# Kernel tuning notes

Hardware: AMD Instinct MI355X
Metric: run time of the kernel (lower is better)

Reference implementation:

```python
import jax, jax.numpy as jnp
import numpy as np
from jax import lax

B, N, C = 4, 16384, 256
NH, HD = 8, 32          # num_heads, head_dim
SR = 4                  # spatial reduction ratio
LMAX = 6144             # max per-batch query length (static pad size)
QLENS = np.array([2048, 6144, 3072, 5120], dtype=np.int32)
TQ = int(QLENS.sum())   # 16384 total ragged queries
SCALE = HD ** -0.5


def setup_inputs() -> dict:
    key = jax.random.key(0)
    ks = jax.random.split(key, 6)
    w = lambda k, s: jax.random.normal(k, s, jnp.float32) * 0.02
    return {
        "x": jax.random.normal(ks[0], (B, N, C), jnp.float32),
        "q": jax.random.normal(ks[1], (TQ, C), jnp.float32),
        "H": 128,
        "W": 128,
        "q_lengths": jnp.asarray(QLENS),
        "w_q": w(ks[2], (C, C)),        # stored [in, out] (= torch W.T)
        "w_kv": w(ks[3], (C, 2 * C)),
        "sr_w": w(ks[4], (C, C, SR, SR)),  # OIHW
        "sr_b": jnp.zeros((C,), jnp.float32),
        "ln_g": jnp.ones((C,), jnp.float32),
        "ln_b": jnp.zeros((C,), jnp.float32),
        "proj_w": w(ks[5], (C, C)),
        "proj_b": jnp.zeros((C,), jnp.float32),
    }


def reference(x, q, H, W, q_lengths, w_q, w_kv, sr_w, sr_b, ln_g, ln_b, proj_w, proj_b):
    # q projection -> per-head ragged queries [NH, TQ, HD]
    qh = (q @ w_q).reshape(TQ, NH, HD).transpose(1, 0, 2)

    # spatial reduction of KV source: conv(k=SR, stride=SR) + LayerNorm
    x_ = x.transpose(0, 2, 1).reshape(B, C, H, W)
    x_ = lax.conv_general_dilated(x_, sr_w, (SR, SR), "VALID",
                                  dimension_numbers=("NCHW", "OIHW", "NCHW"))
    x_ = x_ + sr_b[None, :, None, None]
    x_ = x_.reshape(B, C, -1).transpose(0, 2, 1)  # [B, Nkv, C]
    mu = x_.mean(-1, keepdims=True)
    var = ((x_ - mu) ** 2).mean(-1, keepdims=True)
    x_ = (x_ - mu) * lax.rsqrt(var + 1e-5) * ln_g + ln_b

    # kv projection -> [NH, B, Nkv, HD] each
    kv = (x_ @ w_kv).reshape(B, -1, 2, NH, HD)
    k = kv[:, :, 0].transpose(2, 0, 1, 3)
    v = kv[:, :, 1].transpose(2, 0, 1, 3)

    # ragged -> padded layout for the variable-length attention
    batch_ids = jnp.repeat(jnp.arange(B), q_lengths, total_repeat_length=TQ)
    offsets = jnp.cumsum(q_lengths) - q_lengths
    pos = jnp.arange(TQ) - offsets[batch_ids]
    qp = jnp.zeros((NH, B, LMAX, HD), qh.dtype).at[:, batch_ids, pos].set(qh)

    # per-batch attention over reduced keys (padded rows are discarded below)
    attn = jax.nn.softmax(jnp.einsum("hbld,hbkd->hblk", qp, k) * SCALE, axis=-1)
    op = jnp.einsum("hblk,hbkd->hbld", attn, v)

    # gather valid ragged outputs back: [NH, TQ, HD] -> [TQ, C]
    o = op[:, batch_ids, pos].transpose(1, 0, 2).reshape(TQ, C)
    return o @ proj_w + proj_b
```

## Files before the change

kernel.cpp:

```cpp
#include <hip/hip_runtime.h>
#include <hip/hip_bf16.h>


using bf16 = __hip_bfloat16;
using f32x4 = __attribute__((ext_vector_type(4))) float;
using bf16x8 = __attribute__((ext_vector_type(8))) short;

#define DEVINL __device__ __forceinline__
#define AS1 __attribute__((address_space(1)))
#define AS3 __attribute__((address_space(3)))

DEVINL f32x4 mfma16(bf16x8 a, bf16x8 b, f32x4 c) {
    return __builtin_amdgcn_mfma_f32_16x16x32_bf16(a, b, c, 0, 0, 0);
}

DEVINL unsigned short f2bf(float f) {
    union { float f; unsigned u; } x; x.f = f;
    unsigned u = x.u;
    u += 0x7fffu + ((u >> 16) & 1u);
    return (unsigned short)(u >> 16);
}

DEVINL unsigned pk_rtz(float a, float b) {
    return __builtin_amdgcn_perm(__float_as_uint(b), __float_as_uint(a), 0x07060302u);
}

DEVINL float ex2(float x) { return __builtin_amdgcn_exp2f(x); }

DEVINL void gl16(const bf16* g, bf16* l) {
    __builtin_amdgcn_global_load_lds(
        (const AS1 void*)(unsigned long long)(uintptr_t)g,
        (AS3 void*)(unsigned)(uintptr_t)l, 16, 0, 0);
}
DEVINL void gl16f(const float* g, float* l) {
    __builtin_amdgcn_global_load_lds(
        (const AS1 void*)(unsigned long long)(uintptr_t)g,
        (AS3 void*)(unsigned)(uintptr_t)l, 16, 0, 0);
}

__global__ __launch_bounds__(256) void prep_kernel(
    const float* __restrict__ w_q, const float* __restrict__ w_kv,
    const float* __restrict__ proj_w, const float* __restrict__ sr_w,
    const float* __restrict__ q,
    bf16* __restrict__ wqT, bf16* __restrict__ wkvT, bf16* __restrict__ wprT,
    bf16* __restrict__ wcv, bf16* __restrict__ q_bf)
{
    const int bb = blockIdx.x;
    if (bb < 256) {
        int idx = bb * 256 + threadIdx.x;
        int k = idx & 255, n = idx >> 8;
        wqT[idx] = __float2bfloat16(w_q[k * 256 + n]);
    } else if (bb < 768) {
        int idx = (bb - 256) * 256 + threadIdx.x;
        int k = idx & 255, n = idx >> 8;
        wkvT[idx] = __float2bfloat16(w_kv[k * 512 + n]);
    } else if (bb < 1024) {
        int idx = (bb - 768) * 256 + threadIdx.x;
        int k = idx & 255, n = idx >> 8;
        wprT[idx] = __float2bfloat16(proj_w[k * 256 + n]);
    } else if (bb < 5120) {
        int idx = (bb - 1024) * 256 + threadIdx.x;
        int o = idx >> 12, rest = idx & 4095, dydx = rest >> 8, c = rest & 255;
        wcv[idx] = __float2bfloat16(sr_w[((o << 8) + c) * 16 + dydx]);
    } else {
        int i = (bb - 5120) * 256 + threadIdx.x;
        float4 a = ((const float4*)q)[i * 2];
        float4 b = ((const float4*)q)[i * 2 + 1];
        uint4 u;
        u.x = f2bf(a.x) | ((unsigned)f2bf(a.y) << 16);
        u.y = f2bf(a.z) | ((unsigned)f2bf(a.w) << 16);
        u.z = f2bf(b.x) | ((unsigned)f2bf(b.y) << 16);
        u.w = f2bf(b.z) | ((unsigned)f2bf(b.w) << 16);
        ((uint4*)q_bf)[i] = u;
    }
}

template<int EMODE>
__global__ __launch_bounds__(256, 4) void gemm_kernel(
    const bf16* __restrict__ A, const bf16* __restrict__ WT,
    const float* __restrict__ bias,
    bf16* __restrict__ outb, float* __restrict__ outf, bf16* __restrict__ out2,
    int M, int N, int K, int KS)
{
    __shared__ alignas(16) bf16 As[2][64 * 64];
    __shared__ alignas(16) bf16 Bs[2][64 * 64];
    const int cpx = gridDim.x >> 3;
    const int bx = (blockIdx.x & 7) * cpx + (blockIdx.x >> 3);
    const int ntn = N >> 6;
    const int tm = bx / ntn, tn = bx % ntn;
    const int tid = threadIdx.x, lane = tid & 63, wid = tid >> 6;
    const int l15 = lane & 15, g = lane >> 4;
    const int wm = (wid >> 1) << 5, wn = (wid & 1) << 5;
    f32x4 acc[2][2] = {};

    int r_[2], cs_[2];
#pragma unroll
    for (int j = 0; j < 2; ++j) {
        int idx = (wid * 2 + j) * 64 + lane;
        r_[j] = idx >> 3;
        cs_[j] = ((idx & 7) ^ (r_[j] & 7)) << 3;
    }
    const bf16* Arow = &A[(size_t)(tm * 64) * K];
    const bf16* Brow = &WT[(size_t)(tn * 64) * K];

    const int kbeg = blockIdx.y * KS;
    const int nsteps = KS >> 6;

    auto stage = [&](int buf, int k0) {
#pragma unroll
        for (int j = 0; j < 2; ++j) {
            gl16(Arow + (size_t)r_[j] * K + (k0 + cs_[j]), &As[buf][(wid * 2 + j) * 512]);
            gl16(Brow + (size_t)r_[j] * K + (k0 + cs_[j]), &Bs[buf][(wid * 2 + j) * 512]);
        }
    };

    stage(0, kbeg);
    __syncthreads();

    for (int t = 0; t < nsteps; ++t) {
        const int buf = t & 1;
        if (t + 1 < nsteps) stage(buf ^ 1, kbeg + (t + 1) * 64);
#pragma unroll
        for (int kk = 0; kk < 2; ++kk) {
            const int sw = l15 & 7;
            const int co = ((kk * 4 + g) ^ sw) << 3;
            bf16x8 a0 = *(const bf16x8*)&As[buf][(wm + l15) * 64 + co];
            bf16x8 a1 = *(const bf16x8*)&As[buf][(wm + 16 + l15) * 64 + co];
            bf16x8 b0 = *(const bf16x8*)&Bs[buf][(wn + l15) * 64 + co];
            bf16x8 b1 = *(const bf16x8*)&Bs[buf][(wn + 16 + l15) * 64 + co];
            acc[0][0] = mfma16(a0, b0, acc[0][0]);
            acc[0][1] = mfma16(a0, b1, acc[0][1]);
            acc[1][0] = mfma16(a1, b0, acc[1][0]);
            acc[1][1] = mfma16(a1, b1, acc[1][1]);
        }
        __syncthreads();
    }

    const float qscale = 0.1767766953f * 1.4426950409f;
#pragma unroll
    for (int mi = 0; mi < 2; ++mi)
#pragma unroll
    for (int ni = 0; ni < 2; ++ni)
#pragma unroll
    for (int r = 0; r < 4; ++r) {
        int row = tm * 64 + wm + mi * 16 + g * 4 + r;
        int col = tn * 64 + wn + ni * 16 + l15;
        float v = acc[mi][ni][r];
        if constexpr (EMODE == 0) {
            outb[(size_t)row * 256 + col] = __float2bfloat16(v * qscale);
        } else if constexpr (EMODE == 1) {
            outf[(size_t)row * 256 + col] = v + bias[col];
        } else if constexpr (EMODE == 2) {
            int bb = row >> 10, key = row & 1023;
            if (col < 256) {
                int hh = col >> 5, d = col & 31;
                outb[(size_t)(((bb << 3) + hh) * 1024 + key) * 32 + d] = __float2bfloat16(v);
            } else {
                int d = col - 256;
                int c = key & 31;
                int pos = (((c >> 2) & 3) << 3) + ((c >> 4) << 2) + (c & 3);
                int keyp = (key & ~31) | pos;
                out2[(size_t)(((bb << 3) + (d >> 5)) * 32 + (d & 31)) * 1024 + keyp] =
                    __float2bfloat16(v);
            }
        }
    }
}

__global__ __launch_bounds__(1024, 4) void conv_gemm_kernel(
    const float* __restrict__ X, const bf16* __restrict__ WT,
    const float* __restrict__ bias, float* __restrict__ outf)
{
    __shared__ alignas(16) float Af[2][2][64 * 64];
    __shared__ alignas(16) bf16 Bs[2][2][64 * 64];
    const int K = 4096;
    const int bx = (blockIdx.x & 7) * 32 + (blockIdx.x >> 3);
    const int tm = bx >> 2, tn = bx & 3;
    const int tid = threadIdx.x, lane = tid & 63, wid = tid >> 6;
    const int grp = wid >> 3, wg = wid & 7;
    const int l15 = lane & 15, g = lane >> 4;
    const int wm = (wg >> 1) << 4, wn = (wg & 1) << 5;
    f32x4 acc[2] = {};

    size_t laneoffA[2];
#pragma unroll
    for (int j = 0; j < 2; ++j) {
        int rr = (wg * 2 + j) * 4 + (lane >> 4);
        int pr = tm * 64 + rr;
        int b = pr >> 10, pi = pr & 1023;
        int ii = pi >> 5, jj = pi & 31;
        int c16 = lane & 15;
        int c16s = ((((c16 >> 1) ^ (rr & 7)) << 1) | (c16 & 1));
        laneoffA[j] = ((size_t)((b << 14) + (ii << 2) * 128 + (jj << 2))) * 256
                      + c16s * 4;
    }
    const int rB = wg * 8 + (lane >> 3);
    const int csB = ((lane & 7) ^ (rB & 7)) << 3;
    const bf16* BrowP = &WT[(size_t)(tn * 64 + rB) * K + csB];

    const int kbeg = grp << 11;

    auto stage = [&](int buf, int t) {
        const int k0 = kbeg + t * 64;
        const int dydx = k0 >> 8;
        const int stepoff = ((dydx >> 2) * 128 + (dydx & 3)) * 256 + (k0 & 255);
#pragma unroll
        for (int j = 0; j < 2; ++j)
            gl16f(X + laneoffA[j] + stepoff, &Af[grp][buf][(wg * 2 + j) * 256]);
        gl16(BrowP + k0, &Bs[grp][buf][wg * 512]);
    };

    stage(0, 0);
    __syncthreads();

    for (int t = 0; t < 32; ++t) {
        const int buf = t & 1;
        if (t + 1 < 32) stage(buf ^ 1, t + 1);
#pragma unroll
        for (int kk = 0; kk < 2; ++kk) {
            const int sw = l15 & 7;
            const int uo = ((kk * 4 + g) ^ sw) << 3;
            const float* ap = &Af[grp][buf][(wm + l15) * 64 + uo];
            float4 lo = *(const float4*)ap;
            float4 hi = *(const float4*)(ap + 4);
            uint4 au;
            au.x = pk_rtz(lo.x, lo.y);  au.y = pk_rtz(lo.z, lo.w);
            au.z = pk_rtz(hi.x, hi.y);  au.w = pk_rtz(hi.z, hi.w);
            union { uint4 u; bf16x8 v; } ac; ac.u = au;
            bf16x8 b0 = *(const bf16x8*)&Bs[grp][buf][(wn + l15) * 64 + uo];
            bf16x8 b1 = *(const bf16x8*)&Bs[grp][buf][(wn + 16 + l15) * 64 + uo];
            acc[0] = mfma16(ac.v, b0, acc[0]);
            acc[1] = mfma16(ac.v, b1, acc[1]);
        }
        __syncthreads();
    }

    {
        float* red = &Af[grp][0][0];
#pragma unroll
        for (int ni = 0; ni < 2; ++ni)
#pragma unroll
        for (int r = 0; r < 4; ++r)
            red[(wm + g * 4 + r) * 64 + wn + ni * 16 + l15] = acc[ni][r];
    }
    __syncthreads();
    {
        const int e = tid << 2;
        const float4 s0 = *(const float4*)&Af[0][0][e];
        const float4 s1 = *(const float4*)&Af[1][0][e];
        const int row = e >> 6, col = e & 63;
        const float4 bv = *(const float4*)&bias[tn * 64 + col];
        float4 o;
        o.x = s0.x + s1.x + bv.x;
        o.y = s0.y + s1.y + bv.y;
        o.z = s0.z + s1.z + bv.z;
        o.w = s0.w + s1.w + bv.w;
        *(float4*)&outf[(size_t)(tm * 64 + row) * 256 + tn * 64 + col] = o;
    }
}

__global__ __launch_bounds__(256) void ln_kernel(const float* __restrict__ xr,
                                                 const float* __restrict__ gw,
                                                 const float* __restrict__ bw,
                                                 bf16* __restrict__ out) {
    int row = blockIdx.x * 4 + (threadIdx.x >> 6);
    int lane = threadIdx.x & 63;
    const float4 v = *(const float4*)&xr[(size_t)row * 256 + lane * 4];

    float s = v.x + v.y + v.z + v.w;
#pragma unroll
    for (int m = 1; m < 64; m <<= 1) s += __shfl_xor(s, m, 64);
    float mu = s * 0.00390625f;
    float d0 = v.x - mu, d1 = v.y - mu, d2 = v.z - mu, d3 = v.w - mu;
    float qv = d0 * d0 + d1 * d1 + d2 * d2 + d3 * d3;
#pragma unroll
    for (int m = 1; m < 64; m <<= 1) qv += __shfl_xor(qv, m, 64);
    float rstd = rsqrtf(qv * 0.00390625f + 1e-5f);
    const float4 gg = *(const float4*)&gw[lane * 4];
    const float4 bb = *(const float4*)&bw[lane * 4];
    uint2 u;
    u.x = f2bf(d0 * rstd * gg.x + bb.x) | ((unsigned)f2bf(d1 * rstd * gg.y + bb.y) << 16);
    u.y = f2bf(d2 * rstd * gg.z + bb.z) | ((unsigned)f2bf(d3 * rstd * gg.w + bb.w) << 16);
    *(uint2*)&out[(size_t)row * 256 + lane * 4] = u;
}

__global__ __launch_bounds__(256, 4) void attn_kernel(
    const bf16* __restrict__ qh, const bf16* __restrict__ kh,
    const bf16* __restrict__ vt, bf16* __restrict__ obf)
{
    __shared__ alignas(16) bf16 Kl[2][128 * 32];
    __shared__ alignas(16) bf16 Vl[2][32 * 128];
    const int bid = blockIdx.x;
    const int h = bid & 7;
    const int tile = bid >> 3;
    const int row0 = tile << 7;
    const int b = (row0 < 2048) ? 0 : (row0 < 8192) ? 1 : (row0 < 11264) ? 2 : 3;
    const int tid = threadIdx.x, lane = tid & 63, w = tid >> 6;
    const int l15 = lane & 15, g = lane >> 4;
    const int qbase = row0 + (w << 5);
    const int bh = (b << 3) + h;

    bf16x8 qfA = *(const bf16x8*)&qh[(size_t)(qbase + l15) * 256 + h * 32 + g * 8];
    bf16x8 qfB = *(const bf16x8*)&qh[(size_t)(qbase + 16 + l15) * 256 + h * 32 + g * 8];

    bf16x8 ones;
    {
        unsigned ov = (l15 == 0) ? 0x3f803f80u : 0u;
        unsigned* op = (unsigned*)&ones;
        op[0] = ov; op[1] = ov; op[2] = ov; op[3] = ov;
    }

    f32x4 o0A = {0.f,0.f,0.f,0.f}, o1A = o0A, o2A = o0A;
    f32x4 o0B = o0A, o1B = o0A, o2B = o0A;
    const f32x4 z = {0.f, 0.f, 0.f, 0.f};

    const int skey = lane >> 2;
    const int skc  = (lane & 3) ^ (skey & 3);
    const int svd  = lane >> 4;
    const int svc  = lane & 15;
    const bf16* kbase = kh + (size_t)bh * 1024 * 32;
    const bf16* vbase = vt + (size_t)bh * 32 * 1024;

    auto stage = [&](int buf, int kb) {
        if (w < 2) {
#pragma unroll
            for (int jj = 0; jj < 4; ++jj) {
                int j = w * 4 + jj;
                int key = (j << 4) + skey;
                gl16(kbase + (size_t)(kb + key) * 32 + (skc << 3), &Kl[buf][j * 512]);
            }
        } else {
#pragma unroll
            for (int jj = 0; jj < 4; ++jj) {
                int j = (w - 2) * 4 + jj;
                int d = (j << 2) + svd;
                gl16(vbase + (size_t)d * 1024 + kb + ((svc ^ (d & 7)) << 3),
                     &Vl[buf][j * 512]);
            }
        }
    };

    stage(0, 0);
    __syncthreads();

    const int kc = g ^ (l15 & 3);
    const int vsw = l15 & 7;

    for (int t = 0; t < 8; ++t) {
        const int buf = t & 1;
        if (t < 7) stage(buf ^ 1, (t + 1) << 7);
#pragma unroll
        for (int s = 0; s < 4; ++s) {
            bf16x8 k0 = *(const bf16x8*)&Kl[buf][((s << 5) + l15) * 32 + (kc << 3)];
            bf16x8 k1 = *(const bf16x8*)&Kl[buf][((s << 5) + 16 + l15) * 32 + (kc << 3)];
            bf16x8 v0 = *(const bf16x8*)&Vl[buf][(l15 << 7) + ((((s << 2) + g) ^ vsw) << 3)];
            bf16x8 v1 = *(const bf16x8*)&Vl[buf][((16 + l15) << 7) + ((((s << 2) + g) ^ vsw) << 3)];

            f32x4 s0A = mfma16(k0, qfA, z);
            f32x4 s1A = mfma16(k1, qfA, z);
            f32x4 s0B = mfma16(k0, qfB, z);
            f32x4 s1B = mfma16(k1, qfB, z);

            uint4 pAu, pBu;
            pAu.x = pk_rtz(ex2(s0A[0]), ex2(s0A[1]));
            pAu.y = pk_rtz(ex2(s0A[2]), ex2(s0A[3]));
            pAu.z = pk_rtz(ex2(s1A[0]), ex2(s1A[1]));
            pAu.w = pk_rtz(ex2(s1A[2]), ex2(s1A[3]));
            pBu.x = pk_rtz(ex2(s0B[0]), ex2(s0B[1]));
            pBu.y = pk_rtz(ex2(s0B[2]), ex2(s0B[3]));
            pBu.z = pk_rtz(ex2(s1B[0]), ex2(s1B[1]));
            pBu.w = pk_rtz(ex2(s1B[2]), ex2(s1B[3]));
            union { uint4 u; bf16x8 v; } cA, cB;
            cA.u = pAu; cB.u = pBu;

            o0A = mfma16(cA.v, v0, o0A);
            o1A = mfma16(cA.v, v1, o1A);
            o2A = mfma16(cA.v, ones, o2A);
            o0B = mfma16(cB.v, v0, o0B);
            o1B = mfma16(cB.v, v1, o1B);
            o2B = mfma16(cB.v, ones, o2B);
        }
        __syncthreads();
    }

#pragma unroll
    for (int r = 0; r < 4; ++r) {
        float invA = 1.f / __shfl(o2A[r], g << 4, 64);
        float invB = 1.f / __shfl(o2B[r], g << 4, 64);
        size_t orowA = (size_t)(qbase + (g << 2) + r) * 256 + h * 32;
        size_t orowB = (size_t)(qbase + 16 + (g << 2) + r) * 256 + h * 32;
        obf[orowA + l15]      = __float2bfloat16(o0A[r] * invA);
        obf[orowA + 16 + l15] = __float2bfloat16(o1A[r] * invA);
        obf[orowB + l15]      = __float2bfloat16(o0B[r] * invB);
        obf[orowB + 16 + l15] = __float2bfloat16(o1B[r] * invB);
    }
}


extern "C" void kernel_launch(void* const* d_in, const int* in_sizes, int n_in,
                              void* d_out, int out_size, void* d_ws, size_t ws_size,
                              hipStream_t stream)
{
    const float* x      = (const float*)d_in[0];
    const float* q      = (const float*)d_in[1];
    const float* w_q    = (const float*)d_in[5];
    const float* w_kv   = (const float*)d_in[6];
    const float* sr_w   = (const float*)d_in[7];
    const float* sr_b   = (const float*)d_in[8];
    const float* ln_g   = (const float*)d_in[9];
    const float* ln_b   = (const float*)d_in[10];
    const float* proj_w = (const float*)d_in[11];
    const float* proj_b = (const float*)d_in[12];

    char* w = (char*)d_ws;
    bf16* q_bf = (bf16*)(w + 0);
    bf16* qh   = (bf16*)(w + 8388608);
    bf16* wqT  = (bf16*)(w + 16777216);
    bf16* wkvT = (bf16*)(w + 16908288);
    bf16* wprT = (bf16*)(w + 17170432);
    bf16* wcv  = (bf16*)(w + 17301504);
    bf16* xln  = (bf16*)(w + 19398656);
    bf16* kh   = (bf16*)(w + 21495808);
    bf16* vt   = (bf16*)(w + 23592960);
    bf16* obf  = (bf16*)(w + 25690112);
    float* xr  = (float*)(w + 34078720);
    float* out = (float*)d_out;

    prep_kernel<<<7168, 256, 0, stream>>>(w_q, w_kv, proj_w, sr_w, q,
                                          wqT, wkvT, wprT, wcv, q_bf);
    gemm_kernel<0><<<1024, 256, 0, stream>>>(q_bf, wqT, nullptr, qh, nullptr, nullptr,
                                             16384, 256, 256, 256);
    conv_gemm_kernel<<<256, 1024, 0, stream>>>(x, wcv, sr_b, xr);
    ln_kernel<<<1024, 256, 0, stream>>>(xr, ln_g, ln_b, xln);
    gemm_kernel<2><<<512, 256, 0, stream>>>(xln, wkvT, nullptr, kh, nullptr, vt,
                                            4096, 512, 256, 256);
    attn_kernel<<<1024, 256, 0, stream>>>(qh, kh, vt, obf);
    gemm_kernel<1><<<1024, 256, 0, stream>>>(obf, wprT, proj_b, nullptr, out, nullptr,
                                             16384, 256, 256, 256);
}
```

Measured before the change: 95.33 us.

## Split-K conv GEMM into 8 slices with partial sums reduced in LayerNorm

The conv-as-GEMM kernel changes from 256 blocks of 1024 threads, which split K in two and reduced in shared memory, to 2048 blocks of 256 threads. Each block computes a 64x64 tile over one of 8 K-slices with a 32-wide K step and writes fp32 partials to workspace. The LayerNorm kernel now sums the 8 partials, adds the conv bias, then normalizes. This raises parallelism and occupancy on the many-CU GPU, at the cost of about 32MB of extra partial-sum traffic written and read back.

```diff
diff --git a/kernel.cpp b/kernel.cpp
--- a/kernel.cpp
+++ b/kernel.cpp
@@ -167,105 +167,107 @@
     }
 }
 
-__global__ __launch_bounds__(1024, 4) void conv_gemm_kernel(
+__global__ __launch_bounds__(256, 6) void conv_gemm_kernel(
     const float* __restrict__ X, const bf16* __restrict__ WT,
-    const float* __restrict__ bias, float* __restrict__ outf)
+    float* __restrict__ partials)
 {
-    __shared__ alignas(16) float Af[2][2][64 * 64];
-    __shared__ alignas(16) bf16 Bs[2][2][64 * 64];
+    __shared__ alignas(16) float Af[2][64 * 32];
+    __shared__ alignas(16) bf16 Bs[2][64 * 32];
     const int K = 4096;
-    const int bx = (blockIdx.x & 7) * 32 + (blockIdx.x >> 3);
-    const int tm = bx >> 2, tn = bx & 3;
+    const int swz = (blockIdx.x & 7) * 256 + (blockIdx.x >> 3);
+    const int combo = swz >> 6;
+    const int tm = swz & 63;
+    const int tn = combo >> 3, slice = combo & 7;
     const int tid = threadIdx.x, lane = tid & 63, wid = tid >> 6;
-    const int grp = wid >> 3, wg = wid & 7;
     const int l15 = lane & 15, g = lane >> 4;
-    const int wm = (wg >> 1) << 4, wn = (wg & 1) << 5;
-    f32x4 acc[2] = {};
+    const int wm = (wid >> 1) << 5, wn = (wid & 1) << 5;
+    f32x4 acc[2][2] = {};
 
     size_t laneoffA[2];
 #pragma unroll
     for (int j = 0; j < 2; ++j) {
-        int rr = (wg * 2 + j) * 4 + (lane >> 4);
+        int call = wid * 2 + j;
+        int rr = call * 8 + (lane >> 3);
         int pr = tm * 64 + rr;
         int b = pr >> 10, pi = pr & 1023;
         int ii = pi >> 5, jj = pi & 31;
-        int c16 = lane & 15;
-        int c16s = ((((c16 >> 1) ^ (rr & 7)) << 1) | (c16 & 1));
-        laneoffA[j] = ((size_t)((b << 14) + (ii << 2) * 128 + (jj << 2))) * 256
-                      + c16s * 4;
-    }
-    const int rB = wg * 8 + (lane >> 3);
-    const int csB = ((lane & 7) ^ (rB & 7)) << 3;
-    const bf16* BrowP = &WT[(size_t)(tn * 64 + rB) * K + csB];
-
-    const int kbeg = grp << 11;
+        int c16 = lane & 7;
+        int sc = (((c16 >> 1) ^ (rr & 3)) << 1) | (c16 & 1);
+        laneoffA[j] = ((size_t)((b << 14) + (ii << 2) * 128 + (jj << 2))) * 256 + sc * 4;
+    }
+    const int rB = wid * 16 + (lane >> 2);
+    const int scB = ((lane & 3) ^ (rB & 3)) << 3;
+    const bf16* BrowP = &WT[(size_t)(tn * 64 + rB) * K + scB];
+
+    const int kbeg = slice << 9;
 
     auto stage = [&](int buf, int t) {
-        const int k0 = kbeg + t * 64;
+        const int k0 = kbeg + t * 32;
         const int dydx = k0 >> 8;
         const int stepoff = ((dydx >> 2) * 128 + (dydx & 3)) * 256 + (k0 & 255);
 #pragma unroll
         for (int j = 0; j < 2; ++j)
-            gl16f(X + laneoffA[j] + stepoff, &Af[grp][buf][(wg * 2 + j) * 256]);
-        gl16(BrowP + k0, &Bs[grp][buf][wg * 512]);
+            gl16f(X + laneoffA[j] + stepoff, &Af[buf][(wid * 2 + j) * 256]);
+        gl16(BrowP + k0, &Bs[buf][wid * 512]);
     };
 
     stage(0, 0);
     __syncthreads();
 
-    for (int t = 0; t < 32; ++t) {
+    for (int t = 0; t < 16; ++t) {
         const int buf = t & 1;
-        if (t + 1 < 32) stage(buf ^ 1, t + 1);
-#pragma unroll
-        for (int kk = 0; kk < 2; ++kk) {
-            const int sw = l15 & 7;
-            const int uo = ((kk * 4 + g) ^ sw) << 3;
-            const float* ap = &Af[grp][buf][(wm + l15) * 64 + uo];
-            float4 lo = *(const float4*)ap;
-            float4 hi = *(const float4*)(ap + 4);
-            uint4 au;
-            au.x = pk_rtz(lo.x, lo.y);  au.y = pk_rtz(lo.z, lo.w);
-            au.z = pk_rtz(hi.x, hi.y);  au.w = pk_rtz(hi.z, hi.w);
-            union { uint4 u; bf16x8 v; } ac; ac.u = au;
-            bf16x8 b0 = *(const bf16x8*)&Bs[grp][buf][(wn + l15) * 64 + uo];
-            bf16x8 b1 = *(const bf16x8*)&Bs[grp][buf][(wn + 16 + l15) * 64 + uo];
-            acc[0] = mfma16(ac.v, b0, acc[0]);
-            acc[1] = mfma16(ac.v, b1, acc[1]);
+        if (t + 1 < 16) stage(buf ^ 1, t + 1);
+        {
+            const int sw = l15 & 3;
+            const int ao = (g ^ sw) << 3;
+            const float* ap0 = &Af[buf][(wm + l15) * 32 + ao];
+            const float* ap1 = &Af[buf][(wm + 16 + l15) * 32 + ao];
+            float4 lo0 = *(const float4*)ap0, hi0 = *(const float4*)(ap0 + 4);
+            float4 lo1 = *(const float4*)ap1, hi1 = *(const float4*)(ap1 + 4);
+            uint4 a0u, a1u;
+            a0u.x = pk_rtz(lo0.x, lo0.y);  a0u.y = pk_rtz(lo0.z, lo0.w);
+            a0u.z = pk_rtz(hi0.x, hi0.y);  a0u.w = pk_rtz(hi0.z, hi0.w);
+            a1u.x = pk_rtz(lo1.x, lo1.y);  a1u.y = pk_rtz(lo1.z, lo1.w);
+            a1u.z = pk_rtz(hi1.x, hi1.y);  a1u.w = pk_rtz(hi1.z, hi1.w);
+            union { uint4 u; bf16x8 v; } a0c, a1c; a0c.u = a0u; a1c.u = a1u;
+            bf16x8 b0 = *(const bf16x8*)&Bs[buf][(wn + l15) * 32 + ao];
+            bf16x8 b1 = *(const bf16x8*)&Bs[buf][(wn + 16 + l15) * 32 + ao];
+            acc[0][0] = mfma16(a0c.v, b0, acc[0][0]);
+            acc[0][1] = mfma16(a0c.v, b1, acc[0][1]);
+            acc[1][0] = mfma16(a1c.v, b0, acc[1][0]);
+            acc[1][1] = mfma16(a1c.v, b1, acc[1][1]);
         }
         __syncthreads();
     }
 
-    {
-        float* red = &Af[grp][0][0];
-#pragma unroll
-        for (int ni = 0; ni < 2; ++ni)
-#pragma unroll
-        for (int r = 0; r < 4; ++r)
-            red[(wm + g * 4 + r) * 64 + wn + ni * 16 + l15] = acc[ni][r];
-    }
-    __syncthreads();
-    {
-        const int e = tid << 2;
-        const float4 s0 = *(const float4*)&Af[0][0][e];
-        const float4 s1 = *(const float4*)&Af[1][0][e];
-        const int row = e >> 6, col = e & 63;
-        const float4 bv = *(const float4*)&bias[tn * 64 + col];
-        float4 o;
-        o.x = s0.x + s1.x + bv.x;
-        o.y = s0.y + s1.y + bv.y;
-        o.z = s0.z + s1.z + bv.z;
-        o.w = s0.w + s1.w + bv.w;
-        *(float4*)&outf[(size_t)(tm * 64 + row) * 256 + tn * 64 + col] = o;
-    }
-}
-
-__global__ __launch_bounds__(256) void ln_kernel(const float* __restrict__ xr,
+#pragma unroll
+    for (int mi = 0; mi < 2; ++mi)
+#pragma unroll
+    for (int ni = 0; ni < 2; ++ni)
+#pragma unroll
+    for (int r = 0; r < 4; ++r) {
+        int row = tm * 64 + wm + mi * 16 + g * 4 + r;
+        int col = tn * 64 + wn + ni * 16 + l15;
+        partials[((size_t)slice * 4096 + row) * 256 + col] = acc[mi][ni][r];
+    }
+}
+
+__global__ __launch_bounds__(256) void ln_kernel(const float* __restrict__ pp,
+                                                 const float* __restrict__ cb,
                                                  const float* __restrict__ gw,
                                                  const float* __restrict__ bw,
                                                  bf16* __restrict__ out) {
     int row = blockIdx.x * 4 + (threadIdx.x >> 6);
     int lane = threadIdx.x & 63;
-    const float4 v = *(const float4*)&xr[(size_t)row * 256 + lane * 4];
+    const size_t base = (size_t)row * 256 + lane * 4;
+    float4 v = *(const float4*)&pp[base];
+#pragma unroll
+    for (int s = 1; s < 8; ++s) {
+        const float4 t = *(const float4*)&pp[(size_t)s * (4096 * 256) + base];
+        v.x += t.x; v.y += t.y; v.z += t.z; v.w += t.w;
+    }
+    const float4 cbv = *(const float4*)&cb[lane * 4];
+    v.x += cbv.x; v.y += cbv.y; v.z += cbv.z; v.w += cbv.w;
 
     float s = v.x + v.y + v.z + v.w;
 #pragma unroll
@@ -423,15 +425,15 @@
     bf16* kh   = (bf16*)(w + 21495808);
     bf16* vt   = (bf16*)(w + 23592960);
     bf16* obf  = (bf16*)(w + 25690112);
-    float* xr  = (float*)(w + 34078720);
+    float* partials = (float*)(w + 34078720);
     float* out = (float*)d_out;
 
     prep_kernel<<<7168, 256, 0, stream>>>(w_q, w_kv, proj_w, sr_w, q,
                                           wqT, wkvT, wprT, wcv, q_bf);
     gemm_kernel<0><<<1024, 256, 0, stream>>>(q_bf, wqT, nullptr, qh, nullptr, nullptr,
                                              16384, 256, 256, 256);
-    conv_gemm_kernel<<<256, 1024, 0, stream>>>(x, wcv, sr_b, xr);
-    ln_kernel<<<1024, 256, 0, stream>>>(xr, ln_g, ln_b, xln);
+    conv_gemm_kernel<<<2048, 256, 0, stream>>>(x, wcv, partials);
+    ln_kernel<<<1024, 256, 0, stream>>>(partials, sr_b, ln_g, ln_b, xln);
     gemm_kernel<2><<<512, 256, 0, stream>>>(xln, wkvT, nullptr, kh, nullptr, vt,
                                             4096, 512, 256, 256);
     attn_kernel<<<1024, 256, 0, stream>>>(qh, kh, vt, obf);
```

Result: slower. 112.7 us (+18.2%).

## Drop split-K in conv GEMM, use smaller 32x64 tiles with more blocks

Applied to the files above, without the earlier changes.

The conv GEMM previously ran 1024-thread blocks with a two-way split-K, each half covering 2048 of K, followed by an LDS reduction over 64x64 output tiles. It now uses 256-thread blocks over 32x64 tiles that walk the full K=4096 in 64 steps, with 512 blocks and a new k-major swizzled LDS layout. The epilogue writes accumulators straight to global memory with bias, removing the reduction and one barrier. The cost is a longer serial K loop per block and non-vectorized scattered stores, traded for more, smaller blocks and less LDS per block.

```diff
diff --git a/kernel.cpp b/kernel.cpp
--- a/kernel.cpp
+++ b/kernel.cpp
@@ -167,95 +167,92 @@
     }
 }
 
-__global__ __launch_bounds__(1024, 4) void conv_gemm_kernel(
+__global__ __launch_bounds__(256, 4) void conv_gemm_kernel(
     const float* __restrict__ X, const bf16* __restrict__ WT,
     const float* __restrict__ bias, float* __restrict__ outf)
 {
-    __shared__ alignas(16) float Af[2][2][64 * 64];
-    __shared__ alignas(16) bf16 Bs[2][2][64 * 64];
+    __shared__ alignas(16) float Af[2][2048];
+    __shared__ alignas(16) bf16 Bs[2][4096];
     const int K = 4096;
-    const int bx = (blockIdx.x & 7) * 32 + (blockIdx.x >> 3);
-    const int tm = bx >> 2, tn = bx & 3;
+    const int xcd = blockIdx.x & 7, idx = blockIdx.x >> 3;
+    const int tm = xcd * 16 + (idx >> 2), tn = idx & 3;
     const int tid = threadIdx.x, lane = tid & 63, wid = tid >> 6;
-    const int grp = wid >> 3, wg = wid & 7;
     const int l15 = lane & 15, g = lane >> 4;
-    const int wm = (wg >> 1) << 4, wn = (wg & 1) << 5;
+    const int wm = (wid >> 1) << 4, wn = (wid & 1) << 5;
     f32x4 acc[2] = {};
 
     size_t laneoffA[2];
-#pragma unroll
-    for (int j = 0; j < 2; ++j) {
-        int rr = (wg * 2 + j) * 4 + (lane >> 4);
-        int pr = tm * 64 + rr;
+    int ldsoffA[2];
+#pragma unroll
+    for (int jj = 0; jj < 2; ++jj) {
+        int j = wid * 2 + jj;
+        int c = j * 64 + lane;
+        int k4 = c >> 5;
+        int row = (c & 31) ^ (k4 & 7);
+        int pr = tm * 32 + row;
         int b = pr >> 10, pi = pr & 1023;
-        int ii = pi >> 5, jj = pi & 31;
-        int c16 = lane & 15;
-        int c16s = ((((c16 >> 1) ^ (rr & 7)) << 1) | (c16 & 1));
-        laneoffA[j] = ((size_t)((b << 14) + (ii << 2) * 128 + (jj << 2))) * 256
-                      + c16s * 4;
-    }
-    const int rB = wg * 8 + (lane >> 3);
-    const int csB = ((lane & 7) ^ (rB & 7)) << 3;
-    const bf16* BrowP = &WT[(size_t)(tn * 64 + rB) * K + csB];
-
-    const int kbeg = grp << 11;
+        int ii = pi >> 5, jc = pi & 31;
+        laneoffA[jj] = ((size_t)((b << 14) + (ii << 2) * 128 + (jc << 2))) * 256 + k4 * 4;
+        ldsoffA[jj] = j * 256;
+    }
+    const bf16* laneB[2];
+    int ldsoffB[2];
+#pragma unroll
+    for (int jj = 0; jj < 2; ++jj) {
+        int j = wid * 2 + jj;
+        int c = j * 64 + lane;
+        int k8 = c >> 6;
+        int n = (c & 63) ^ (k8 & 7);
+        laneB[jj] = &WT[(size_t)(tn * 64 + n) * K + k8 * 8];
+        ldsoffB[jj] = j * 512;
+    }
 
     auto stage = [&](int buf, int t) {
-        const int k0 = kbeg + t * 64;
+        const int k0 = t * 64;
         const int dydx = k0 >> 8;
         const int stepoff = ((dydx >> 2) * 128 + (dydx & 3)) * 256 + (k0 & 255);
 #pragma unroll
-        for (int j = 0; j < 2; ++j)
-            gl16f(X + laneoffA[j] + stepoff, &Af[grp][buf][(wg * 2 + j) * 256]);
-        gl16(BrowP + k0, &Bs[grp][buf][wg * 512]);
+        for (int jj = 0; jj < 2; ++jj) {
+            gl16f(X + laneoffA[jj] + stepoff, &Af[buf][ldsoffA[jj]]);
+            gl16(laneB[jj] + k0, &Bs[buf][ldsoffB[jj]]);
+        }
     };
 
     stage(0, 0);
     __syncthreads();
 
-    for (int t = 0; t < 32; ++t) {
+    for (int t = 0; t < 64; ++t) {
         const int buf = t & 1;
-        if (t + 1 < 32) stage(buf ^ 1, t + 1);
+        if (t + 1 < 64) stage(buf ^ 1, t + 1);
 #pragma unroll
         for (int kk = 0; kk < 2; ++kk) {
-            const int sw = l15 & 7;
-            const int uo = ((kk * 4 + g) ^ sw) << 3;
-            const float* ap = &Af[grp][buf][(wm + l15) * 64 + uo];
-            float4 lo = *(const float4*)ap;
-            float4 hi = *(const float4*)(ap + 4);
+            const int k4lo = kk * 8 + g * 2;
+            const int clo = k4lo * 32 + ((wm + l15) ^ (k4lo & 7));
+            const int chi = (k4lo + 1) * 32 + ((wm + l15) ^ ((k4lo + 1) & 7));
+            float4 lo = *(const float4*)&Af[buf][clo * 4];
+            float4 hi = *(const float4*)&Af[buf][chi * 4];
             uint4 au;
             au.x = pk_rtz(lo.x, lo.y);  au.y = pk_rtz(lo.z, lo.w);
             au.z = pk_rtz(hi.x, hi.y);  au.w = pk_rtz(hi.z, hi.w);
             union { uint4 u; bf16x8 v; } ac; ac.u = au;
-            bf16x8 b0 = *(const bf16x8*)&Bs[grp][buf][(wn + l15) * 64 + uo];
-            bf16x8 b1 = *(const bf16x8*)&Bs[grp][buf][(wn + 16 + l15) * 64 + uo];
+            const int k8 = kk * 4 + g;
+            const int cb0 = k8 * 64 + ((wn + l15) ^ (k8 & 7));
+            const int cb1 = k8 * 64 + ((wn + 16 + l15) ^ (k8 & 7));
+            bf16x8 b0 = *(const bf16x8*)&Bs[buf][cb0 * 8];
+            bf16x8 b1 = *(const bf16x8*)&Bs[buf][cb1 * 8];
             acc[0] = mfma16(ac.v, b0, acc[0]);
             acc[1] = mfma16(ac.v, b1, acc[1]);
         }
         __syncthreads();
     }
 
-    {
-        float* red = &Af[grp][0][0];
-#pragma unroll
-        for (int ni = 0; ni < 2; ++ni)
-#pragma unroll
-        for (int r = 0; r < 4; ++r)
-            red[(wm + g * 4 + r) * 64 + wn + ni * 16 + l15] = acc[ni][r];
-    }
-    __syncthreads();
-    {
-        const int e = tid << 2;
-        const float4 s0 = *(const float4*)&Af[0][0][e];
-        const float4 s1 = *(const float4*)&Af[1][0][e];
-        const int row = e >> 6, col = e & 63;
-        const float4 bv = *(const float4*)&bias[tn * 64 + col];
-        float4 o;
-        o.x = s0.x + s1.x + bv.x;
-        o.y = s0.y + s1.y + bv.y;
-        o.z = s0.z + s1.z + bv.z;
-        o.w = s0.w + s1.w + bv.w;
-        *(float4*)&outf[(size_t)(tm * 64 + row) * 256 + tn * 64 + col] = o;
+#pragma unroll
+    for (int cf = 0; cf < 2; ++cf)
+#pragma unroll
+    for (int r = 0; r < 4; ++r) {
+        int row = tm * 32 + wm + g * 4 + r;
+        int col = tn * 64 + wn + cf * 16 + l15;
+        outf[(size_t)row * 256 + col] = acc[cf][r] + bias[col];
     }
 }
 
@@ -430,7 +427,7 @@
                                           wqT, wkvT, wprT, wcv, q_bf);
     gemm_kernel<0><<<1024, 256, 0, stream>>>(q_bf, wqT, nullptr, qh, nullptr, nullptr,
                                              16384, 256, 256, 256);
-    conv_gemm_kernel<<<256, 1024, 0, stream>>>(x, wcv, sr_b, xr);
+    conv_gemm_kernel<<<512, 256, 0, stream>>>(x, wcv, sr_b, xr);
     ln_kernel<<<1024, 256, 0, stream>>>(xr, ln_g, ln_b, xln);
     gemm_kernel<2><<<512, 256, 0, stream>>>(xln, wkvT, nullptr, kh, nullptr, vt,
                                             4096, 512, 256, 256);
```

After: 121.6 us. 27.5% more time.
